# Kernel tuning notes

Hardware: AMD Instinct MI355X
Metric: run time of the kernel (lower is better)

Reference implementation:

```python
import jax, jax.numpy as jnp
import numpy as np

N_NODES = 20000
N_EDGES = 640000
FEAT = 128


def setup_inputs() -> dict:
    key = jax.random.key(0)
    k1, k2, k3, k4 = jax.random.split(key, 4)
    x = jax.random.normal(k1, (1, N_NODES, FEAT, 4), dtype=jnp.float32)
    edge_index = jax.random.randint(k2, (2, N_EDGES), 0, N_NODES, dtype=jnp.int64)
    # Linear(in_channels=128, out_channels=128): W [out, in], b [out]
    W = jax.random.normal(k3, (FEAT, FEAT), dtype=jnp.float32) * 0.05
    b = jax.random.normal(k4, (FEAT,), dtype=jnp.float32) * 0.05
    return {"x": x, "edge_index": edge_index, "W": W, "b": b}


def reference(x, edge_index, W, b):
    # x: [B, N, F, T]
    B, N, F, T = x.shape
    # permute -> [B, T, N, F]; Linear over feature dim (out == in == F)
    h = jnp.einsum('bnft,of->btno', x, W) + b          # [B, T, N, F]
    h = h.reshape(B * T, N, F)                          # flatten batch*time
    src = edge_index[0]  # message source (x_j)
    dst = edge_index[1]  # scatter target
    msgs = h[:, src, :]                                 # [B*T, E, F] gather
    # scatter-max per target node (PyG aggr='max'); vmap over batch*time
    agg = jax.vmap(lambda m: jax.ops.segment_max(m, dst, num_segments=N))(msgs)
    # nodes with no incoming edges: segment_max yields -inf -> 0 (PyG fill)
    agg = jnp.where(jnp.isneginf(agg), jnp.zeros_like(agg), agg)
    out = agg.reshape(B, T, N, F).transpose(0, 2, 3, 1)  # [B, N, F, T]
    return out
```

## Files before the change

kernel.cpp:

```cpp
#include <hip/hip_runtime.h>
#include <hip/hip_bf16.h>
#include <stdint.h>

#define N_NODES 20000
#define N_EDGES 640000
#define FEAT 128
#define CAPD 128
#define NPHASE 8
#define CNTSTRIDE 16

typedef __attribute__((ext_vector_type(8))) short bf16x8;
typedef __attribute__((ext_vector_type(4))) float f32x4;

__device__ __forceinline__ unsigned pkbf16(float lo, float hi) {
  __hip_bfloat162 p = __float22bfloat162_rn(make_float2(lo, hi));
  return *reinterpret_cast<unsigned*>(&p);
}

__device__ __forceinline__ unsigned short enc16(float f) {
  unsigned a = __float_as_uint(f);
  unsigned b = (a + 0x7FFFu + ((a >> 16) & 1u)) >> 16;
  unsigned s = (unsigned)((int)a >> 31);
  return (unsigned short)((b ^ 0x8000u) ^ (s & 0x7FFFu));
}

__device__ __forceinline__ float dec16(unsigned e) {
  unsigned b = (e & 0x8000u) ? (e ^ 0x8000u) : (e ^ 0xFFFFu);
  return __uint_as_float(b << 16);
}

__device__ __forceinline__ void pmax(unsigned& a, unsigned v) {
  asm("v_pk_max_u16 %0, %0, %1" : "+v"(a) : "v"(v));
}

#define PMX4(v)                                              \
  do {                                                       \
    pmax(a0, (v).x); pmax(a1, (v).y);                        \
    pmax(a2, (v).z); pmax(a3, (v).w);                        \
  } while (0)

__global__ void init_kernel(const float* __restrict__ W,
                            unsigned short* __restrict__ Wbf,
                            int* __restrict__ cnt) {
  int i = blockIdx.x * 256 + threadIdx.x;
  if (i < N_NODES * CNTSTRIDE) cnt[i] = 0;
  if (i < FEAT * FEAT / 2) {
    float2 w = ((const float2*)W)[i];
    ((unsigned*)Wbf)[i] = pkbf16(w.x, w.y);
  }
}

__global__ __launch_bounds__(512) void gemm_scatter_kernel(
    const float4* __restrict__ x, const unsigned short* __restrict__ Wbf,
    const float* __restrict__ b, uint4* __restrict__ h,
    const int* __restrict__ ei, int* __restrict__ cnt,
    unsigned short* __restrict__ csr) {
  __shared__ __align__(16) unsigned short sm[17408 / 2];
  const int tid = threadIdx.x;
  const int bid = blockIdx.x;
  const int m3 = bid % 3;

  if (m3 == 2) {
    const int base = (bid / 3) * 1024;
#pragma unroll
    for (int r = 0; r < 2; ++r) {
      int e = base + r * 512 + tid;
      int src = ei[e];
      int dst = ei[N_EDGES + e];
      int pos = atomicAdd(&cnt[dst * CNTSTRIDE], 1);
      if (pos < CAPD) csr[(size_t)dst * CAPD + pos] = (unsigned short)src;
    }
    return;
  }

  const int tile = (bid / 3) * 2 + m3;
  const int n0 = tile * 16;

  const int e0 = tid, e1 = tid + 512;
  const int na = e0 >> 6, fa = e0 & 63;
  const int nb = e1 >> 6, fb = e1 & 63;
  float4 a0 = x[(size_t)(n0 + na) * 128 + 2 * fa];
  float4 c0 = x[(size_t)(n0 + na) * 128 + 2 * fa + 1];
  float4 a1 = x[(size_t)(n0 + nb) * 128 + 2 * fb];
  float4 c1 = x[(size_t)(n0 + nb) * 128 + 2 * fb + 1];

  ((unsigned*)sm)[(0 * 16 + na) * 68 + fa] = pkbf16(a0.x, c0.x);
  ((unsigned*)sm)[(1 * 16 + na) * 68 + fa] = pkbf16(a0.y, c0.y);
  ((unsigned*)sm)[(2 * 16 + na) * 68 + fa] = pkbf16(a0.z, c0.z);
  ((unsigned*)sm)[(3 * 16 + na) * 68 + fa] = pkbf16(a0.w, c0.w);
  ((unsigned*)sm)[(0 * 16 + nb) * 68 + fb] = pkbf16(a1.x, c1.x);
  ((unsigned*)sm)[(1 * 16 + nb) * 68 + fb] = pkbf16(a1.y, c1.y);
  ((unsigned*)sm)[(2 * 16 + nb) * 68 + fb] = pkbf16(a1.z, c1.z);
  ((unsigned*)sm)[(3 * 16 + nb) * 68 + fb] = pkbf16(a1.w, c1.w);

  __syncthreads();

  const int wv = tid >> 6;
  const int l = tid & 63;
  const int col = l & 15;
  const int quad = l >> 4;
  const int t = wv & 3;
  const int osh = wv >> 2;

  f32x4 acc[4];
#pragma unroll
  for (int os = 0; os < 4; ++os) {
    float bv = b[(osh * 4 + os) * 16 + col];
    acc[os] = (f32x4){bv, bv, bv, bv};
  }

#pragma unroll
  for (int k = 0; k < 4; ++k) {
    bf16x8 af = *(const bf16x8*)&sm[(t * 16 + col) * 136 + k * 32 + quad * 8];
#pragma unroll
    for (int os = 0; os < 4; ++os) {
      bf16x8 bfv =
          *(const bf16x8*)&Wbf[((osh * 4 + os) * 16 + col) * 128 + k * 32 + quad * 8];
      acc[os] = __builtin_amdgcn_mfma_f32_16x16x32_bf16(af, bfv, acc[os], 0, 0, 0);
    }
  }

  __syncthreads();

#pragma unroll
  for (int os = 0; os < 4; ++os) {
#pragma unroll
    for (int r = 0; r < 4; ++r) {
      sm[(quad * 4 + r) * 520 + ((osh * 4 + os) * 16 + col) * 4 + t] = enc16(acc[os][r]);
    }
  }
  __syncthreads();

#pragma unroll
  for (int it = 0; it < 2; ++it) {
    int e = tid + it * 512;
    int n = e >> 6, q = e & 63;
    uint4 v = *(const uint4*)&sm[n * 520 + q * 8];
    h[(size_t)(n0 + n) * 64 + q] = v;
  }
}

__global__ __launch_bounds__(256) void agg_kernel(
    const uint4* __restrict__ h, const int* __restrict__ cnt,
    const unsigned short* __restrict__ csr, float4* __restrict__ out) {
  __shared__ __align__(16) unsigned short sidx[32][136];
  const int bid = blockIdx.x;
  const int p = bid & 7;
  const int grp = bid >> 3;
  const int n0 = grp * 32;
  const int tid = threadIdx.x;

  {
    int r = tid >> 3;
    int q = tid & 7;
    const uint4* srow = (const uint4*)(csr + (size_t)(n0 + r) * CAPD);
    *(uint4*)&sidx[r][q * 8] = srow[q];
    *(uint4*)&sidx[r][(q + 8) * 8] = srow[q + 8];
  }
  __syncthreads();

  const int w = tid >> 6;
  const int lane = tid & 63;
  const int g = lane >> 3;
  const int oq = lane & 7;
  const int n = n0 + w * 8 + g;

  int deg = cnt[n * CNTSTRIDE];
  deg = deg > CAPD ? CAPD : deg;

  const unsigned short* myrow = sidx[w * 8 + g];
  int idx0 = (deg > 0) ? (int)myrow[0] : 0;

  int dmax = deg;
#pragma unroll
  for (int d = 8; d <= 32; d <<= 1) {
    int o = __shfl_xor(dmax, d);
    dmax = o > dmax ? o : dmax;
  }
  dmax = __builtin_amdgcn_readfirstlane(dmax);

  unsigned a0 = 0x007F007Fu, a1 = a0, a2 = a0, a3 = a0;
  const char* hb = (const char*)h;
  const unsigned pb = (((unsigned)p * 8 + oq) << 4);

  for (int jb = 0; jb < dmax; jb += 8) {
    uint4 iv = *(const uint4*)&myrow[jb];
    int e0 = (int)(iv.x & 0xFFFFu), e1 = (int)(iv.x >> 16);
    int e2 = (int)(iv.y & 0xFFFFu), e3 = (int)(iv.y >> 16);
    int e4 = (int)(iv.z & 0xFFFFu), e5 = (int)(iv.z >> 16);
    int e6 = (int)(iv.w & 0xFFFFu), e7 = (int)(iv.w >> 16);
    e0 = (jb + 0 < deg) ? e0 : idx0;
    e1 = (jb + 1 < deg) ? e1 : idx0;
    e2 = (jb + 2 < deg) ? e2 : idx0;
    e3 = (jb + 3 < deg) ? e3 : idx0;
    e4 = (jb + 4 < deg) ? e4 : idx0;
    e5 = (jb + 5 < deg) ? e5 : idx0;
    e6 = (jb + 6 < deg) ? e6 : idx0;
    e7 = (jb + 7 < deg) ? e7 : idx0;
    uint4 v0 = *(const uint4*)(hb + (((unsigned)e0 << 10) + pb));
    uint4 v1 = *(const uint4*)(hb + (((unsigned)e1 << 10) + pb));
    uint4 v2 = *(const uint4*)(hb + (((unsigned)e2 << 10) + pb));
    uint4 v3 = *(const uint4*)(hb + (((unsigned)e3 << 10) + pb));
    uint4 v4 = *(const uint4*)(hb + (((unsigned)e4 << 10) + pb));
    uint4 v5 = *(const uint4*)(hb + (((unsigned)e5 << 10) + pb));
    uint4 v6 = *(const uint4*)(hb + (((unsigned)e6 << 10) + pb));
    uint4 v7 = *(const uint4*)(hb + (((unsigned)e7 << 10) + pb));
    PMX4(v0); PMX4(v1); PMX4(v2); PMX4(v3);
    PMX4(v4); PMX4(v5); PMX4(v6); PMX4(v7);
  }

  float4 o0, o1;
  if (deg == 0) {
    o0 = make_float4(0.f, 0.f, 0.f, 0.f);
    o1 = o0;
  } else {
    o0 = make_float4(dec16(a0 & 0xFFFFu), dec16(a0 >> 16),
                     dec16(a1 & 0xFFFFu), dec16(a1 >> 16));
    o1 = make_float4(dec16(a2 & 0xFFFFu), dec16(a2 >> 16),
                     dec16(a3 & 0xFFFFu), dec16(a3 >> 16));
  }
  out[(size_t)n * 128 + p * 16 + oq * 2] = o0;
  out[(size_t)n * 128 + p * 16 + oq * 2 + 1] = o1;
}

extern "C" void kernel_launch(void* const* d_in, const int* in_sizes, int n_in,
                              void* d_out, int out_size, void* d_ws, size_t ws_size,
                              hipStream_t stream) {
  const float* x = (const float*)d_in[0];
  const int* ei = (const int*)d_in[1];
  const float* W = (const float*)d_in[2];
  const float* b = (const float*)d_in[3];
  float* out = (float*)d_out;

  char* ws = (char*)d_ws;
  uint4* h = (uint4*)ws;
  int* cnt = (int*)(ws + 20480000);
  unsigned short* csr = (unsigned short*)(ws + 21760000);
  unsigned short* Wbf = (unsigned short*)(ws + 26880000);

  init_kernel<<<(N_NODES * CNTSTRIDE + 255) / 256, 256, 0, stream>>>(W, Wbf, cnt);
  gemm_scatter_kernel<<<1875, 512, 0, stream>>>((const float4*)x, Wbf, b, h,
                                                ei, cnt, csr);
  agg_kernel<<<(N_NODES / 32) * NPHASE, 256, 0, stream>>>(h, cnt, csr, (float4*)out);
}
```

Before: 168.2 us.

## Partition edge CSR into eight sub-buckets and fold weight conversion into GEMM

Edge scatter blocks now write into one of eight partitioned count/CSR arrays, each capped at 24 slots per node, chosen by block index. This spreads atomic contention and shrinks the per-node CSR footprint. The aggregation kernel merges the partitions with an in-warp prefix sum into a shared index row. The separate init kernel is replaced by a memset of the counts, and each GEMM block converts the full fp32 W to bf16 in LDS itself. That adds redundant W reads per block and extra LDS use, which may lower occupancy. The per-partition cap could drop edges for very skewed degree distributions.

```diff
diff --git a/kernel.cpp b/kernel.cpp
--- a/kernel.cpp
+++ b/kernel.cpp
@@ -5,9 +5,9 @@
 #define N_NODES 20000
 #define N_EDGES 640000
 #define FEAT 128
-#define CAPD 128
+#define CAP8 24
+#define NPART 8
 #define NPHASE 8
-#define CNTSTRIDE 16
 
 typedef __attribute__((ext_vector_type(8))) short bf16x8;
 typedef __attribute__((ext_vector_type(4))) float f32x4;
@@ -39,42 +39,50 @@
     pmax(a2, (v).z); pmax(a3, (v).w);                        \
   } while (0)
 
-__global__ void init_kernel(const float* __restrict__ W,
-                            unsigned short* __restrict__ Wbf,
-                            int* __restrict__ cnt) {
-  int i = blockIdx.x * 256 + threadIdx.x;
-  if (i < N_NODES * CNTSTRIDE) cnt[i] = 0;
-  if (i < FEAT * FEAT / 2) {
-    float2 w = ((const float2*)W)[i];
-    ((unsigned*)Wbf)[i] = pkbf16(w.x, w.y);
-  }
-}
-
 __global__ __launch_bounds__(512) void gemm_scatter_kernel(
-    const float4* __restrict__ x, const unsigned short* __restrict__ Wbf,
+    const float4* __restrict__ x, const float* __restrict__ W,
     const float* __restrict__ b, uint4* __restrict__ h,
     const int* __restrict__ ei, int* __restrict__ cnt,
     unsigned short* __restrict__ csr) {
   __shared__ __align__(16) unsigned short sm[17408 / 2];
+  __shared__ __align__(16) unsigned short Wlds[128 * 136];
   const int tid = threadIdx.x;
   const int bid = blockIdx.x;
   const int m3 = bid % 3;
 
   if (m3 == 2) {
     const int base = (bid / 3) * 1024;
+    const int vx = bid & 7;
+    int* mycnt = cnt + vx * N_NODES;
+    unsigned short* mycsr = csr + (size_t)vx * N_NODES * CAP8;
 #pragma unroll
     for (int r = 0; r < 2; ++r) {
       int e = base + r * 512 + tid;
       int src = ei[e];
       int dst = ei[N_EDGES + e];
-      int pos = atomicAdd(&cnt[dst * CNTSTRIDE], 1);
-      if (pos < CAPD) csr[(size_t)dst * CAPD + pos] = (unsigned short)src;
+      int pos = atomicAdd(&mycnt[dst], 1);
+      if (pos < CAP8) mycsr[(size_t)dst * CAP8 + pos] = (unsigned short)src;
     }
     return;
   }
 
   const int tile = (bid / 3) * 2 + m3;
   const int n0 = tile * 16;
+
+  {
+    const float4* Wv = (const float4*)W;
+    const int o = tid >> 2;
+    const int q0 = (tid & 3) * 8;
+    float4 wa[8];
+#pragma unroll
+    for (int q = 0; q < 8; ++q) wa[q] = Wv[o * 32 + q0 + q];
+    unsigned* wrow = (unsigned*)&Wlds[o * 136] + (tid & 3) * 16;
+#pragma unroll
+    for (int q = 0; q < 8; ++q) {
+      wrow[2 * q] = pkbf16(wa[q].x, wa[q].y);
+      wrow[2 * q + 1] = pkbf16(wa[q].z, wa[q].w);
+    }
+  }
 
   const int e0 = tid, e1 = tid + 512;
   const int na = e0 >> 6, fa = e0 & 63;
@@ -115,7 +123,7 @@
 #pragma unroll
     for (int os = 0; os < 4; ++os) {
       bf16x8 bfv =
-          *(const bf16x8*)&Wbf[((osh * 4 + os) * 16 + col) * 128 + k * 32 + quad * 8];
+          *(const bf16x8*)&Wlds[((osh * 4 + os) * 16 + col) * 136 + k * 32 + quad * 8];
       acc[os] = __builtin_amdgcn_mfma_f32_16x16x32_bf16(af, bfv, acc[os], 0, 0, 0);
     }
   }
@@ -143,7 +151,8 @@
 __global__ __launch_bounds__(256) void agg_kernel(
     const uint4* __restrict__ h, const int* __restrict__ cnt,
     const unsigned short* __restrict__ csr, float4* __restrict__ out) {
-  __shared__ __align__(16) unsigned short sidx[32][136];
+  __shared__ __align__(16) unsigned short sidx[32][200];
+  __shared__ int degs[32];
   const int bid = blockIdx.x;
   const int p = bid & 7;
   const int grp = bid >> 3;
@@ -151,11 +160,21 @@
   const int tid = threadIdx.x;
 
   {
-    int r = tid >> 3;
-    int q = tid & 7;
-    const uint4* srow = (const uint4*)(csr + (size_t)(n0 + r) * CAPD);
-    *(uint4*)&sidx[r][q * 8] = srow[q];
-    *(uint4*)&sidx[r][(q + 8) * 8] = srow[q + 8];
+    const int vx = tid & 7;
+    const int r = tid >> 3;
+    const int nn = n0 + r;
+    int c = cnt[vx * N_NODES + nn];
+    c = c > CAP8 ? CAP8 : c;
+    int s = c;
+#pragma unroll
+    for (int d = 1; d < 8; d <<= 1) {
+      int tt = __shfl_up(s, d, 8);
+      if (vx >= d) s += tt;
+    }
+    int off = s - c;
+    if (vx == 7) degs[r] = s;
+    const unsigned short* bsrc = csr + ((size_t)vx * N_NODES + nn) * CAP8;
+    for (int k = 0; k < c; ++k) sidx[r][off + k] = bsrc[k];
   }
   __syncthreads();
 
@@ -165,9 +184,7 @@
   const int oq = lane & 7;
   const int n = n0 + w * 8 + g;
 
-  int deg = cnt[n * CNTSTRIDE];
-  deg = deg > CAPD ? CAPD : deg;
-
+  const int deg = degs[w * 8 + g];
   const unsigned short* myrow = sidx[w * 8 + g];
   int idx0 = (deg > 0) ? (int)myrow[0] : 0;
 
@@ -235,11 +252,10 @@
   char* ws = (char*)d_ws;
   uint4* h = (uint4*)ws;
   int* cnt = (int*)(ws + 20480000);
-  unsigned short* csr = (unsigned short*)(ws + 21760000);
-  unsigned short* Wbf = (unsigned short*)(ws + 26880000);
-
-  init_kernel<<<(N_NODES * CNTSTRIDE + 255) / 256, 256, 0, stream>>>(W, Wbf, cnt);
-  gemm_scatter_kernel<<<1875, 512, 0, stream>>>((const float4*)x, Wbf, b, h,
+  unsigned short* csr = (unsigned short*)(ws + 21120000);
+
+  hipMemsetAsync(cnt, 0, NPART * N_NODES * sizeof(int), stream);
+  gemm_scatter_kernel<<<1875, 512, 0, stream>>>((const float4*)x, W, b, h,
                                                 ei, cnt, csr);
   agg_kernel<<<(N_NODES / 32) * NPHASE, 256, 0, stream>>>(h, cnt, csr, (float4*)out);
 }
```

Measured after the change: 171.8 us. 1.02x slower.
